# Optimization experiments

Hardware: AMD Instinct MI355X
Metric: run time of the kernel (lower is better)

Reference implementation:

```python
import jax, jax.numpy as jnp
import numpy as np

STRIDE = 16.0
PRE_NMS_TOP_N = 6000
POST_NMS_TOP_N = 1000
NMS_THRESH = 0.7
MIN_SIZE = 0.0
BBOX_XFORM_CLIP = float(np.log(1000.0 / 16.0))

# ---- Detectron-style anchor generation (numpy, setup-time only) ----

def _whctrs(a):
    w = a[2] - a[0] + 1
    h = a[3] - a[1] + 1
    return w, h, a[0] + 0.5 * (w - 1), a[1] + 0.5 * (h - 1)

def _mkanchors(ws, hs, xc, yc):
    return np.stack([xc - 0.5 * (ws - 1), yc - 0.5 * (hs - 1),
                     xc + 0.5 * (ws - 1), yc + 0.5 * (hs - 1)], axis=1)

def _ratio_enum(a, ratios):
    w, h, xc, yc = _whctrs(a)
    size = w * h
    ws = np.round(np.sqrt(size / ratios))
    hs = np.round(ws * ratios)
    return _mkanchors(ws, hs, xc, yc)

def _scale_enum(a, scales):
    w, h, xc, yc = _whctrs(a)
    return _mkanchors(w * scales, h * scales, xc, yc)

def generate_anchors(stride=16.0, sizes=(32, 64, 128, 256, 512), aspect_ratios=(0.5, 1.0, 2.0)):
    scales = np.array(sizes, dtype=np.float64) / stride
    ratios = np.array(aspect_ratios, dtype=np.float64)
    base = np.array([1, 1, stride, stride], dtype=np.float64) - 1
    ra = _ratio_enum(base, ratios)
    return np.vstack([_scale_enum(ra[i], scales) for i in range(ra.shape[0])]).astype(np.float32)


def conv2d(x, w, b, pad):
    y = jax.lax.conv_general_dilated(x, w, (1, 1), [(pad, pad), (pad, pad)],
                                     dimension_numbers=('NCHW', 'OIHW', 'NCHW'))
    return y + b[None, :, None, None]


def _proposals_one(scores, deltas, iminfo, anchors):
    # scores: (A,H,W) sigmoid probs; deltas: (4A,H,W); iminfo: [im_h, im_w, im_scale]
    A, H, W = scores.shape
    gx, gy = jnp.meshgrid(jnp.arange(W, dtype=scores.dtype) * STRIDE,
                          jnp.arange(H, dtype=scores.dtype) * STRIDE)
    shifts = jnp.stack([gx, gy, gx, gy], axis=-1)  # (H,W,4)
    all_anchors = (shifts[:, :, None, :] + anchors[None, None]).reshape(-1, 4)  # (H*W*A,4)
    sc = scores.transpose(1, 2, 0).reshape(-1)      # (H*W*A,)  anchor-minor, matches Detectron
    dl = deltas.transpose(1, 2, 0).reshape(-1, 4)   # (H*W*A,4)

    top_sc, idx = jax.lax.top_k(sc, PRE_NMS_TOP_N)  # descending scores
    boxes = all_anchors[idx]
    d = dl[idx]

    # bbox_transform decode (weights = 1)
    widths = boxes[:, 2] - boxes[:, 0] + 1.0
    heights = boxes[:, 3] - boxes[:, 1] + 1.0
    ctr_x = boxes[:, 0] + 0.5 * widths
    ctr_y = boxes[:, 1] + 0.5 * heights
    dx, dy = d[:, 0], d[:, 1]
    dw = jnp.minimum(d[:, 2], BBOX_XFORM_CLIP)
    dh = jnp.minimum(d[:, 3], BBOX_XFORM_CLIP)
    pcx = dx * widths + ctr_x
    pcy = dy * heights + ctr_y
    pw = jnp.exp(dw) * widths
    ph = jnp.exp(dh) * heights
    x1 = pcx - 0.5 * pw
    y1 = pcy - 0.5 * ph
    x2 = pcx + 0.5 * pw - 1.0
    y2 = pcy + 0.5 * ph - 1.0

    im_h, im_w, im_scale = iminfo[0], iminfo[1], iminfo[2]
    x1 = jnp.clip(x1, 0.0, im_w - 1.0)
    y1 = jnp.clip(y1, 0.0, im_h - 1.0)
    x2 = jnp.clip(x2, 0.0, im_w - 1.0)
    y2 = jnp.clip(y2, 0.0, im_h - 1.0)

    ws = x2 - x1 + 1.0
    hs = y2 - y1 + 1.0
    xc = x1 + ws / 2.0
    yc = y1 + hs / 2.0
    ms = MIN_SIZE * im_scale
    valid = (ws >= ms) & (hs >= ms) & (xc < im_w) & (yc < im_h)

    boxes_s = jnp.stack([x1, y1, x2, y2], axis=1)

    # greedy NMS over score-sorted boxes (invalid boxes start suppressed)
    areas = ws * hs
    ix1 = jnp.maximum(x1[:, None], x1[None, :])
    iy1 = jnp.maximum(y1[:, None], y1[None, :])
    ix2 = jnp.minimum(x2[:, None], x2[None, :])
    iy2 = jnp.minimum(y2[:, None], y2[None, :])
    iw = jnp.maximum(ix2 - ix1 + 1.0, 0.0)
    ih = jnp.maximum(iy2 - iy1 + 1.0, 0.0)
    inter = iw * ih
    iou = inter / (areas[:, None] + areas[None, :] - inter)

    N = PRE_NMS_TOP_N
    rng = jnp.arange(N)

    def body(i, keep):
        sup = (iou[i] > NMS_THRESH) & (rng > i)
        return jnp.where(keep[i], keep & ~sup, keep)

    keep = jax.lax.fori_loop(0, N, body, valid)

    final_sc = jnp.where(keep, jnp.where(valid, top_sc, -1.0), -1.0)
    out_sc, kidx = jax.lax.top_k(final_sc, POST_NMS_TOP_N)
    out_boxes = boxes_s[kidx]
    return out_boxes, out_sc


def setup_inputs() -> dict:
    key = jax.random.key(0)
    ks = jax.random.split(key, 5)
    B, C, H, W = 2, 512, 50, 84
    A = 15  # 5 sizes x 3 aspect ratios
    x = jax.random.normal(ks[0], (B, C, H, W), jnp.float32)
    conv_w = 0.01 * jax.random.normal(ks[1], (C, C, 3, 3), jnp.float32)
    conv_b = jnp.zeros((C,), jnp.float32)
    cls_w = 0.01 * jax.random.normal(ks[2], (A, C, 1, 1), jnp.float32)
    cls_b = jnp.zeros((A,), jnp.float32)
    bbox_w = 0.01 * jax.random.normal(ks[3], (4 * A, C, 1, 1), jnp.float32)
    bbox_b = jnp.zeros((4 * A,), jnp.float32)
    anchors = jnp.asarray(generate_anchors(STRIDE))
    im_info = jnp.array([[800.0, 1333.0, 1.6], [800.0, 1333.0, 1.6]], jnp.float32)
    return {'x': x, 'im_info': im_info, 'conv_w': conv_w, 'conv_b': conv_b,
            'cls_w': cls_w, 'cls_b': cls_b, 'bbox_w': bbox_w, 'bbox_b': bbox_b,
            'anchors': anchors}


def reference(x, im_info, conv_w, conv_b, cls_w, cls_b, bbox_w, bbox_b, anchors):
    h = jax.nn.relu(conv2d(x, conv_w, conv_b, 1))
    rpn_cls_logits = conv2d(h, cls_w, cls_b, 0)        # (B, A, H, W)
    rpn_bbox_pred = conv2d(h, bbox_w, bbox_b, 0)       # (B, 4A, H, W)
    rpn_cls_prob = jax.nn.sigmoid(rpn_cls_logits)      # CLS_ACTIVATION = 'sigmoid'
    boxes, probs = jax.vmap(_proposals_one, in_axes=(0, 0, 0, None))(
        rpn_cls_prob, rpn_bbox_pred, im_info, anchors)  # (B, POST_NMS, 4), (B, POST_NMS)
    B = x.shape[0]
    bidx = jnp.broadcast_to(jnp.arange(B, dtype=boxes.dtype)[:, None, None],
                            (B, POST_NMS_TOP_N, 1))
    rpn_rois = jnp.concatenate([bidx, boxes], axis=-1)  # (B, POST_NMS, 5)
    return rpn_cls_logits, rpn_bbox_pred, rpn_rois, probs
```

## Files before the change

### kernel.cpp

```cpp
#include <hip/hip_runtime.h>
#include <cstdint>
#include <cstddef>

typedef unsigned long long u64;
typedef unsigned int u32;

constexpr int B_ = 2, C_ = 512, H_ = 50, W_ = 84, A_ = 15;
constexpr int HW_ = H_ * W_;
constexpr int NS_ = HW_ * A_;
constexpr int PRE_ = 6000, POST_ = 1000;
constexpr int WORDS_ = 94;
constexpr int NPAD_ = 6016;
constexpr int SORTN_ = 8192;
constexpr double NMS_T = 0.7;
constexpr double CLIP_ = 4.1351665567423556;
constexpr int OUT_ROIS_ = B_ * A_ * HW_ + B_ * 4 * A_ * HW_;
constexpr int OUT_PROBS_ = OUT_ROIS_ + B_ * POST_ * 5;
constexpr int NROUNDS_ = 5;

__global__ void k_init(const float* __restrict__ w, double* __restrict__ wt64,
                       double* __restrict__ h0, double* __restrict__ h1,
                       double* __restrict__ h2, double* __restrict__ h3, int nbuf,
                       u64* __restrict__ mask, u32* __restrict__ selcnt,
                       u32* __restrict__ selhist, u64* __restrict__ selk,
                       u32* __restrict__ seli) {
  int idx = blockIdx.x * 256 + threadIdx.x;
  if (idx < C_ * C_ * 9) {
    int co = idx & 511;
    int r = idx >> 9;
    int k = r % 9;
    int ci = r / 9;
    wt64[idx] = (double)w[(co * C_ + ci) * 9 + k];
  }
  if (idx < B_ * C_ * HW_) {
    h0[idx] = 0.0; h1[idx] = 0.0;
    if (nbuf == 4) { h2[idx] = 0.0; h3[idx] = 0.0; }
  }
  if (idx < B_ * NPAD_ * WORDS_) mask[idx] = 0ull;
  if (idx < 2) selcnt[idx] = 0u;
  if (idx < NROUNDS_ * 2 * 256) selhist[idx] = 0u;
  if (idx < B_ * SORTN_) { selk[idx] = 0ull; seli[idx] = 0xFFFFFFFFu; }
}

template<int QBITS>
__global__ __launch_bounds__(256) void k_conv3(const float* __restrict__ x,
                                               const double* __restrict__ wt64,
                                               double* __restrict__ h0,
                                               double* __restrict__ h1,
                                               double* __restrict__ h2,
                                               double* __restrict__ h3) {
  constexpr int CHUNKS = 128 >> QBITS;
  const int tid = threadIdx.x;
  const int lane = tid & 63;
  const int wid = __builtin_amdgcn_readfirstlane(tid >> 6);
  const int cg = lane % 12;
  const int rowg = lane / 12;
  const bool act = (rowg < 5);
  const int colb = blockIdx.x;
  const int rowb = blockIdx.y;
  const int z = blockIdx.z;
  const int b = z >> (4 + QBITS);
  const int cob = (z >> QBITS) & 15;
  const int q = z & ((1 << QBITS) - 1);
  const int c0 = colb * 12;
  const int rblk = rowb * 10;
  const int col = c0 + cg;
  const int rg5 = act ? rowg : 4;
  const int r0 = rblk + rg5 * 2;
  const int cstart = q * CHUNKS;
  const int bsel = q >> 1;
  double* __restrict__ hp = (bsel == 0) ? h0 : (bsel == 1) ? h1 : (bsel == 2) ? h2 : h3;

  __shared__ double xs[4][14][14];

  double acc[2][8];
#pragma unroll
  for (int j = 0; j < 2; ++j)
#pragma unroll
    for (int c = 0; c < 8; ++c) acc[j][c] = 0.0;

  float xreg[3];
  auto loadX = [&](int cb4) {
#pragma unroll
    for (int k = 0; k < 3; ++k) {
      int s = tid + k * 256;
      float v = 0.f;
      if (s < 672) {
        int ci = s / 168;
        int r168 = s % 168;
        int rr = r168 / 14;
        int cc = r168 % 14;
        int gr = rblk - 1 + rr, gc = c0 - 1 + cc;
        if (gr >= 0 && gr < H_ && gc >= 0 && gc < W_)
          v = x[((b * C_ + cb4 * 4 + ci) * H_ + gr) * W_ + gc];
      }
      xreg[k] = v;
    }
  };
  auto storeX = [&]() {
#pragma unroll
    for (int k = 0; k < 3; ++k) {
      int s = tid + k * 256;
      if (s < 672) {
        int ci = s / 168;
        int r168 = s % 168;
        int rr = r168 / 14;
        int cc = r168 % 14;
        xs[ci][cc][rr] = (double)xreg[k];
      }
    }
  };

  const double* __restrict__ wb = wt64 + (size_t)(cob * 32 + wid * 8);

  loadX(cstart);
  for (int it = 0; it < CHUNKS; ++it) {
    const int cb4 = cstart + it;
    __syncthreads();
    storeX();
    __syncthreads();
    if (it < CHUNKS - 1) loadX(cb4 + 1);
#pragma unroll
    for (int ci = 0; ci < 4; ++ci) {
#pragma unroll
      for (int kx = 0; kx < 3; ++kx) {
        double xv[4];
        const double* xp = &xs[ci][cg + kx][rg5 * 2];
#pragma unroll
        for (int t = 0; t < 4; ++t) xv[t] = xp[t];
#pragma unroll
        for (int ky = 0; ky < 3; ++ky) {
          const double* __restrict__ wp =
              wb + ((size_t)(cb4 * 4 + ci) * 9 + (ky * 3 + kx)) * C_;
#pragma unroll
          for (int c = 0; c < 8; ++c) {
            double wv = wp[c];
            acc[0][c] = fma(xv[ky], wv, acc[0][c]);
            acc[1][c] = fma(xv[ky + 1], wv, acc[1][c]);
          }
        }
      }
    }
  }

  if (act) {
#pragma unroll
    for (int c = 0; c < 8; ++c) {
      int co = cob * 32 + wid * 8 + c;
#pragma unroll
      for (int j = 0; j < 2; ++j) {
        atomicAdd(&hp[((size_t)b * C_ + co) * HW_ + (r0 + j) * W_ + col], acc[j][c]);
      }
    }
  }
}

__global__ __launch_bounds__(256) void k_conv1(const double* __restrict__ h0,
                                               const double* __restrict__ h1,
                                               const double* __restrict__ h2,
                                               const double* __restrict__ h3, int nbuf,
                                               const float* __restrict__ convb,
                                               const float* __restrict__ clsw,
                                               const float* __restrict__ clsb,
                                               const float* __restrict__ bbw,
                                               const float* __restrict__ bbb,
                                               float* __restrict__ out,
                                               double* __restrict__ scores,
                                               double* __restrict__ deltas) {
  const int b = blockIdx.y;
  const int p0 = blockIdx.x * 32;
  const int tid = threadIdx.x;
  const int px = tid & 31, cg = tid >> 5;
  __shared__ double hs[64][32];
  __shared__ double wl[64][80];
  double acc[10];
#pragma unroll
  for (int k = 0; k < 10; ++k) acc[k] = 0.0;
  for (int ci0 = 0; ci0 < C_; ci0 += 64) {
    for (int s = tid; s < 64 * 32; s += 256) {
      int ci = s >> 5, pp = s & 31;
      int p = p0 + pp;
      double v = 0.0;
      if (p < HW_) {
        size_t idx = ((size_t)b * C_ + ci0 + ci) * HW_ + p;
        double hsum = h0[idx] + h1[idx];
        if (nbuf == 4) hsum = hsum + (h2[idx] + h3[idx]);
        v = hsum + (double)convb[ci0 + ci];
        v = v > 0.0 ? v : 0.0;
      }
      hs[ci][pp] = v;
    }
    for (int s = tid; s < 64 * 80; s += 256) {
      int ci = s / 80, c = s % 80;
      double v = 0.0;
      if (c < 15) v = (double)clsw[c * C_ + ci0 + ci];
      else if (c < 75) v = (double)bbw[(c - 15) * C_ + ci0 + ci];
      wl[ci][c] = v;
    }
    __syncthreads();
    for (int ci = 0; ci < 64; ++ci) {
      double xv = hs[ci][px];
#pragma unroll
      for (int k = 0; k < 10; ++k)
        acc[k] = fma(wl[ci][cg * 10 + k], xv, acc[k]);
    }
    __syncthreads();
  }
  int p = p0 + px;
  if (p < HW_) {
#pragma unroll
    for (int k = 0; k < 10; ++k) {
      int c = cg * 10 + k;
      if (c < 15) {
        double z = acc[k] + (double)clsb[c];
        out[(size_t)b * NS_ + c * HW_ + p] = (float)z;
        double s = 1.0 / (1.0 + exp(-z));
        scores[(size_t)b * NS_ + (size_t)p * A_ + c] = s;
      } else if (c < 75) {
        int cbx = c - 15;
        double z = acc[k] + (double)bbb[cbx];
        out[(size_t)B_ * NS_ + (size_t)b * (4 * A_ * HW_) + cbx * HW_ + p] = (float)z;
        deltas[(size_t)b * (4 * NS_) + (size_t)p * (4 * A_) + cbx] = z;
      }
    }
  }
}

__device__ inline u64 compute_prefix(const u32* __restrict__ selhist, int b, int rounds) {
  u64 prefix = 0;
  u32 above = 0;
  for (int rr = 0; rr < rounds; ++rr) {
    const u32* h = selhist + (rr * 2 + b) * 256;
    int shift = 56 - 8 * rr;
    u32 c = above;
    int dsel = 0;
    for (int dd = 255; dd >= 0; --dd) {
      u32 nc = c + h[dd];
      if (nc >= (u32)PRE_) { dsel = dd; break; }
      c = nc;
    }
    prefix |= ((u64)dsel << shift);
    above = c;
  }
  return prefix;
}

__global__ __launch_bounds__(256) void k_hist(const double* __restrict__ scores,
                                              u32* __restrict__ selhist, int r) {
  const int b = blockIdx.y;
  const double* sc = scores + (size_t)b * NS_;
  const int lane = (int)(threadIdx.x & 63);
  const int shift = 56 - 8 * r;
  __shared__ u64 sh_prefix;
  if (threadIdx.x == 0) sh_prefix = (r == 0) ? 0ull : compute_prefix(selhist, b, r);
  __syncthreads();
  const u64 prefix = sh_prefix;
  const u64 himask = (r == 0) ? 0ull : (~0ull << (shift + 8));
  u32* hist = selhist + (r * 2 + b) * 256;
  for (int i = blockIdx.x * 256 + (int)threadIdx.x; i < NS_; i += 64 * 256) {
    u64 k = (u64)__double_as_longlong(sc[i]);
    bool valid = ((k & himask) == (prefix & himask));
    u32 d = (u32)((k >> shift) & 255);
    u64 m = __ballot(valid);
#pragma unroll
    for (int bit = 0; bit < 8; ++bit) {
      u64 bb = __ballot((d >> bit) & 1);
      m &= ((d >> bit) & 1) ? bb : ~bb;
    }
    if (valid && lane == (__ffsll((unsigned long long)m) - 1))
      atomicAdd(&hist[d], (u32)__popcll(m));
  }
}

__global__ __launch_bounds__(256) void k_compact(const double* __restrict__ scores,
                                                 const u32* __restrict__ selhist,
                                                 u32* __restrict__ selcnt,
                                                 u64* __restrict__ selk,
                                                 u32* __restrict__ seli) {
  const int b = blockIdx.y;
  const double* sc = scores + (size_t)b * NS_;
  const int lane = (int)(threadIdx.x & 63);
  __shared__ u64 sh_T;
  if (threadIdx.x == 0) sh_T = compute_prefix(selhist, b, NROUNDS_);
  __syncthreads();
  const u64 T = sh_T;
  for (int i = blockIdx.x * 256 + (int)threadIdx.x; i < NS_; i += 64 * 256) {
    u64 k = (u64)__double_as_longlong(sc[i]);
    bool q = (k >= T);
    u64 bal = __ballot(q);
    if (bal) {
      int leader = __ffsll((unsigned long long)bal) - 1;
      u32 wbase = 0;
      if (lane == leader) wbase = atomicAdd(&selcnt[b], (u32)__popcll(bal));
      wbase = (u32)__shfl((int)wbase, leader);
      if (q) {
        u64 below = (lane == 0) ? 0ull : (~0ull >> (64 - lane));
        u32 pos = wbase + (u32)__popcll(bal & below);
        if (pos < (u32)SORTN_) {
          selk[(size_t)b * SORTN_ + pos] = k;
          seli[(size_t)b * SORTN_ + pos] = (u32)i;
        }
      }
    }
  }
}

__global__ __launch_bounds__(1024) void k_sort(const u64* __restrict__ selk,
                                               const u32* __restrict__ seli,
                                               double* __restrict__ ssc,
                                               u32* __restrict__ sidx) {
  const int b = blockIdx.x;
  __shared__ u64 kk[SORTN_];
  __shared__ u32 vv[SORTN_];
  for (int i = threadIdx.x; i < SORTN_; i += 1024) {
    kk[i] = selk[(size_t)b * SORTN_ + i];
    vv[i] = seli[(size_t)b * SORTN_ + i];
  }
  __syncthreads();
  for (int k = 2; k <= SORTN_; k <<= 1) {
    for (int j = k >> 1; j > 0; j >>= 1) {
      for (int t = threadIdx.x; t < SORTN_; t += 1024) {
        int ixj = t ^ j;
        if (ixj > t) {
          u64 ka = kk[t], kb2 = kk[ixj];
          u32 va = vv[t], vb = vv[ixj];
          bool aBetter = (ka > kb2) || (ka == kb2 && va < vb);
          bool bBetter = (kb2 > ka) || (kb2 == ka && vb < va);
          bool up = (t & k) == 0;
          bool sw = up ? bBetter : aBetter;
          if (sw) {
            kk[t] = kb2; kk[ixj] = ka;
            vv[t] = vb;  vv[ixj] = va;
          }
        }
      }
      __syncthreads();
    }
  }
  for (int i = threadIdx.x; i < PRE_; i += 1024) {
    ssc[(size_t)b * PRE_ + i] = __longlong_as_double((long long)kk[i]);
    sidx[(size_t)b * PRE_ + i] = vv[i];
  }
}

__global__ __launch_bounds__(256) void k_decode(const u32* __restrict__ sidx,
                                                const double* __restrict__ deltas,
                                                const float* __restrict__ anchors,
                                                const float* __restrict__ iminfo,
                                                double* __restrict__ boxes,
                                                double* __restrict__ areas,
                                                u64* __restrict__ vmask) {
#pragma clang fp contract(off)
  const int b = blockIdx.y;
  const int i = blockIdx.x * 256 + (int)threadIdx.x;
  bool valid = false;
  if (i < NPAD_) {
    double x1 = 0, y1 = 0, x2 = 0, y2 = 0, ar = 0;
    if (i < PRE_) {
      u32 idx = sidx[(size_t)b * PRE_ + i];
      int p = (int)idx / A_, a = (int)idx % A_;
      int yy = p / W_, xx = p % W_;
      double sx = xx * 16.0, sy = yy * 16.0;
      double b0 = sx + (double)anchors[a * 4 + 0];
      double b1 = sy + (double)anchors[a * 4 + 1];
      double b2 = sx + (double)anchors[a * 4 + 2];
      double b3 = sy + (double)anchors[a * 4 + 3];
      double wdt = b2 - b0 + 1.0, hgt = b3 - b1 + 1.0;
      double cx = b0 + 0.5 * wdt, cy = b1 + 0.5 * hgt;
      const double* d = deltas + (size_t)b * (4 * NS_) + (size_t)idx * 4;
      double dx = d[0], dy = d[1];
      double dw = d[2] < CLIP_ ? d[2] : CLIP_;
      double dh = d[3] < CLIP_ ? d[3] : CLIP_;
      double pcx = dx * wdt + cx, pcy = dy * hgt + cy;
      double pw = exp(dw) * wdt, ph = exp(dh) * hgt;
      x1 = pcx - 0.5 * pw;
      y1 = pcy - 0.5 * ph;
      x2 = pcx + 0.5 * pw - 1.0;
      y2 = pcy + 0.5 * ph - 1.0;
      double imh = (double)iminfo[b * 3 + 0];
      double imw = (double)iminfo[b * 3 + 1];
      x1 = x1 < 0.0 ? 0.0 : (x1 > imw - 1.0 ? imw - 1.0 : x1);
      y1 = y1 < 0.0 ? 0.0 : (y1 > imh - 1.0 ? imh - 1.0 : y1);
      x2 = x2 < 0.0 ? 0.0 : (x2 > imw - 1.0 ? imw - 1.0 : x2);
      y2 = y2 < 0.0 ? 0.0 : (y2 > imh - 1.0 ? imh - 1.0 : y2);
      double wss = x2 - x1 + 1.0, hss = y2 - y1 + 1.0;
      double xc = x1 + wss / 2.0, yc = y1 + hss / 2.0;
      valid = (wss >= 0.0) && (hss >= 0.0) && (xc < imw) && (yc < imh);
      ar = wss * hss;
    }
    double* bx = boxes + ((size_t)b * NPAD_ + i) * 4;
    bx[0] = x1; bx[1] = y1; bx[2] = x2; bx[3] = y2;
    areas[(size_t)b * NPAD_ + i] = ar;
  }
  u64 bal = __ballot(valid);
  if ((threadIdx.x & 63) == 0) {
    int w = i >> 6;
    if (w < WORDS_) vmask[b * WORDS_ + w] = bal;
  }
}

__global__ __launch_bounds__(256) void k_mask(const double* __restrict__ boxes,
                                              const double* __restrict__ areas,
                                              u64* __restrict__ mask) {
#pragma clang fp contract(off)
  const int b = blockIdx.z;
  const int wc = blockIdx.x;
  const int rq = blockIdx.y;
  if (wc * 64 + 63 <= rq * 256) return;
  const int i = rq * 256 + (int)threadIdx.x;
  __shared__ double cbx[64][4];
  __shared__ double car[64];
  if (threadIdx.x < 64) {
    int sj = wc * 64 + (int)threadIdx.x;
    const double* pj = boxes + ((size_t)b * NPAD_ + sj) * 4;
    cbx[threadIdx.x][0] = pj[0];
    cbx[threadIdx.x][1] = pj[1];
    cbx[threadIdx.x][2] = pj[2];
    cbx[threadIdx.x][3] = pj[3];
    car[threadIdx.x] = areas[(size_t)b * NPAD_ + sj];
  }
  __syncthreads();
  if (i >= PRE_) return;
  int jmax = PRE_ - wc * 64;
  if (jmax > 64) jmax = 64;
  if (wc * 64 + jmax - 1 <= i) return;
  const double* bi = boxes + ((size_t)b * NPAD_ + i) * 4;
  double x1 = bi[0], y1 = bi[1], x2 = bi[2], y2 = bi[3];
  double ai = areas[(size_t)b * NPAD_ + i];
  u64 m = 0;
  for (int j2 = 0; j2 < jmax; ++j2) {
    int j = wc * 64 + j2;
    if (j > i) {
      double ix1 = x1 > cbx[j2][0] ? x1 : cbx[j2][0];
      double iy1 = y1 > cbx[j2][1] ? y1 : cbx[j2][1];
      double ix2 = x2 < cbx[j2][2] ? x2 : cbx[j2][2];
      double iy2 = y2 < cbx[j2][3] ? y2 : cbx[j2][3];
      double iw = ix2 - ix1 + 1.0;
      if (iw < 0.0) iw = 0.0;
      double ih = iy2 - iy1 + 1.0;
      if (ih < 0.0) ih = 0.0;
      double inter = iw * ih;
      double iou = inter / (ai + car[j2] - inter);
      if (iou > NMS_T) m |= (1ull << j2);
    }
  }
  if (m) mask[((size_t)b * NPAD_ + i) * WORDS_ + wc] = m;
}

__global__ __launch_bounds__(64) void k_scan(const u64* __restrict__ mask,
                                             const u64* __restrict__ vmask,
                                             u64* __restrict__ keepm) {
  const int b = blockIdx.x;
  const int lane = (int)threadIdx.x;
  u64 rem0 = ~vmask[b * WORDS_ + lane];
  u64 rem1 = (lane < WORDS_ - 64) ? ~vmask[b * WORDS_ + 64 + lane] : ~0ull;
  const u64* mb = mask + (size_t)b * NPAD_ * WORDS_;
  int kept = 0;
  int Bb = 0;
  u64 dgnext = (lane < 64) ? mb[(size_t)lane * WORDS_ + 0] : 0ull;
  for (; Bb < WORDS_ && kept < POST_; ++Bb) {
    const int base = Bb * 64;
    int lim = PRE_ - base;
    if (lim > 64) lim = 64;
    u64 dg = (lane < lim) ? dgnext : 0ull;
    if (Bb + 1 < WORDS_) {
      int nbase = (Bb + 1) * 64;
      int nlim = PRE_ - nbase;
      if (nlim > 64) nlim = 64;
      dgnext = (lane < nlim) ? mb[(size_t)(nbase + lane) * WORDS_ + (Bb + 1)] : 0ull;
    }
    u64 cur = (Bb < 64) ? __shfl(rem0, Bb) : __shfl(rem1, Bb - 64);
    if (lim < 64) cur |= (~0ull) << lim;
    u64 kb = 0;
    while (cur != ~0ull) {
      int t = __ffsll((unsigned long long)~cur) - 1;
      kb |= 1ull << t;
      cur |= __shfl(dg, t);
      cur |= 1ull << t;
      if (++kept >= POST_) break;
    }
    u64 or0 = 0, or1 = 0;
    u64 k2 = kb;
    while (k2) {
      int t0 = __ffsll((unsigned long long)k2) - 1; k2 &= k2 - 1;
      int t1 = -1, t2 = -1, t3 = -1;
      if (k2) { t1 = __ffsll((unsigned long long)k2) - 1; k2 &= k2 - 1; }
      if (k2) { t2 = __ffsll((unsigned long long)k2) - 1; k2 &= k2 - 1; }
      if (k2) { t3 = __ffsll((unsigned long long)k2) - 1; k2 &= k2 - 1; }
      const u64* m0 = mb + (size_t)(base + t0) * WORDS_;
      u64 a0 = m0[lane];
      u64 a1 = (lane < WORDS_ - 64) ? m0[64 + lane] : 0ull;
      u64 b0 = 0, b1 = 0, c0 = 0, c1 = 0, d0 = 0, d1 = 0;
      if (t1 >= 0) {
        const u64* m1 = mb + (size_t)(base + t1) * WORDS_;
        b0 = m1[lane]; b1 = (lane < WORDS_ - 64) ? m1[64 + lane] : 0ull;
      }
      if (t2 >= 0) {
        const u64* m2 = mb + (size_t)(base + t2) * WORDS_;
        c0 = m2[lane]; c1 = (lane < WORDS_ - 64) ? m2[64 + lane] : 0ull;
      }
      if (t3 >= 0) {
        const u64* m3 = mb + (size_t)(base + t3) * WORDS_;
        d0 = m3[lane]; d1 = (lane < WORDS_ - 64) ? m3[64 + lane] : 0ull;
      }
      or0 |= (a0 | b0) | (c0 | d0);
      or1 |= (a1 | b1) | (c1 | d1);
    }
    rem0 |= or0;
    rem1 |= or1;
    if (lane == 0) keepm[b * WORDS_ + Bb] = kb;
  }
  for (int w = Bb + lane; w < WORDS_; w += 64)
    keepm[b * WORDS_ + w] = 0ull;
}

__global__ __launch_bounds__(256) void k_final(const u64* __restrict__ keepm,
                                               const double* __restrict__ boxes,
                                               const double* __restrict__ ssc,
                                               float* __restrict__ out) {
  const int b = blockIdx.x;
  __shared__ u32 pk[WORDS_ + 1];
  __shared__ u64 km_s[WORDS_];
  for (int w = threadIdx.x; w < WORDS_; w += 256) km_s[w] = keepm[b * WORDS_ + w];
  __syncthreads();
  if (threadIdx.x == 0) {
    u32 a = 0;
    for (int w = 0; w < WORDS_; ++w) {
      pk[w] = a;
      a += (u32)__popcll(km_s[w]);
    }
    pk[WORDS_] = a;
  }
  __syncthreads();
  const u32 K = pk[WORDS_];
  for (int i = threadIdx.x; i < PRE_; i += 256) {
    int w = i >> 6, t = i & 63;
    u64 km = km_s[w];
    u32 before = pk[w] + (u32)__popcll(km & ((1ull << t) - 1ull));
    bool kp = (km >> t) & 1ull;
    int slot = kp ? (int)before : (int)K + (i - (int)before);
    if (slot < POST_) {
      const double* bx = boxes + ((size_t)b * NPAD_ + i) * 4;
      float* ro = out + OUT_ROIS_ + ((size_t)b * POST_ + slot) * 5;
      ro[0] = (float)b;
      ro[1] = (float)bx[0];
      ro[2] = (float)bx[1];
      ro[3] = (float)bx[2];
      ro[4] = (float)bx[3];
      out[OUT_PROBS_ + b * POST_ + slot] = kp ? (float)ssc[(size_t)b * PRE_ + i] : -1.0f;
    }
  }
}

extern "C" void kernel_launch(void* const* d_in, const int* in_sizes, int n_in,
                              void* d_out, int out_size, void* d_ws, size_t ws_size,
                              hipStream_t stream) {
  (void)in_sizes; (void)n_in; (void)out_size;
  const float* x = (const float*)d_in[0];
  const float* iminfo = (const float*)d_in[1];
  const float* convw = (const float*)d_in[2];
  const float* convb = (const float*)d_in[3];
  const float* clsw = (const float*)d_in[4];
  const float* clsb = (const float*)d_in[5];
  const float* bbw = (const float*)d_in[6];
  const float* bbb = (const float*)d_in[7];
  const float* anchors = (const float*)d_in[8];
  float* out = (float*)d_out;

  char* ws = (char*)d_ws;
  size_t off = 0;
  auto alloc = [&](size_t bytes) -> void* {
    void* p = ws + off;
    off += (bytes + 255) & ~(size_t)255;
    return p;
  };
  const size_t HB = (size_t)B_ * C_ * HW_ * 8;
  double* wt64 = (double*)alloc((size_t)C_ * 9 * C_ * 8);
  double* h0 = (double*)alloc(HB);
  double* h1 = (double*)alloc(HB);
  double* scores = (double*)alloc((size_t)B_ * NS_ * 8);
  double* deltas = (double*)alloc((size_t)B_ * NS_ * 4 * 8);
  u64* selk = (u64*)alloc((size_t)B_ * SORTN_ * 8);
  u32* seli = (u32*)alloc((size_t)B_ * SORTN_ * 4);
  double* ssc = (double*)alloc((size_t)B_ * PRE_ * 8);
  u32* sidx = (u32*)alloc((size_t)B_ * PRE_ * 4);
  double* boxes = (double*)alloc((size_t)B_ * NPAD_ * 4 * 8);
  double* areas = (double*)alloc((size_t)B_ * NPAD_ * 8);
  u64* vmask = (u64*)alloc((size_t)B_ * WORDS_ * 8);
  u64* mask = (u64*)alloc((size_t)B_ * NPAD_ * WORDS_ * 8);
  u64* keepm = (u64*)alloc((size_t)B_ * WORDS_ * 8);
  u32* selcnt = (u32*)alloc(2 * 4);
  u32* selhist = (u32*)alloc((size_t)NROUNDS_ * 2 * 256 * 4);

  const bool k8 = (ws_size >= off + 2 * (HB + 256) + 256);
  double* h2 = h0;
  double* h3 = h1;
  int nbuf = 2;
  if (k8) {
    h2 = (double*)alloc(HB);
    h3 = (double*)alloc(HB);
    nbuf = 4;
  }

  k_init<<<(B_ * C_ * HW_ + 255) / 256, 256, 0, stream>>>(
      convw, wt64, h0, h1, h2, h3, nbuf, mask, selcnt, selhist, selk, seli);
  if (k8)
    k_conv3<3><<<dim3(7, 5, 256), 256, 0, stream>>>(x, wt64, h0, h1, h2, h3);
  else
    k_conv3<2><<<dim3(7, 5, 128), 256, 0, stream>>>(x, wt64, h0, h1, h2, h3);
  k_conv1<<<dim3(132, 2), 256, 0, stream>>>(h0, h1, h2, h3, nbuf, convb, clsw, clsb,
                                            bbw, bbb, out, scores, deltas);
  for (int r = 0; r < NROUNDS_; ++r)
    k_hist<<<dim3(64, 2), 256, 0, stream>>>(scores, selhist, r);
  k_compact<<<dim3(64, 2), 256, 0, stream>>>(scores, selhist, selcnt, selk, seli);
  k_sort<<<2, 1024, 0, stream>>>(selk, seli, ssc, sidx);
  k_decode<<<dim3(24, 2), 256, 0, stream>>>(sidx, deltas, anchors, iminfo, boxes, areas, vmask);
  k_mask<<<dim3(94, 24, 2), 256, 0, stream>>>(boxes, areas, mask);
  k_scan<<<2, 64, 0, stream>>>(mask, vmask, keepm);
  k_final<<<2, 256, 0, stream>>>(keepm, boxes, ssc, out);
}
```

Measured before the change: 1.494 ms.

## Replace single-block bitonic sort with parallel rank-counting sort and scatter

The top-K selection sort, which ran as a bitonic sort in one 1024-thread block per image, is replaced by a rank-counting sort. Each candidate's rank is computed by comparing it against a chunk of all other candidates, spread over 8x8 blocks per image, with partial counts combined by atomics and then scattered to sorted positions. This trades a serial-dependent sort on two CUs for more total O(n^2) comparisons spread across many CUs, and it drops the selk/seli padding initialisation.

Result: faster. 1.385 ms (-7.3%).

```diff
diff --git a/kernel.cpp b/kernel.cpp
--- a/kernel.cpp
+++ b/kernel.cpp
@@ -17,13 +17,13 @@
 constexpr int OUT_ROIS_ = B_ * A_ * HW_ + B_ * 4 * A_ * HW_;
 constexpr int OUT_PROBS_ = OUT_ROIS_ + B_ * POST_ * 5;
 constexpr int NROUNDS_ = 5;
+constexpr int JCH_ = 8;
 
 __global__ void k_init(const float* __restrict__ w, double* __restrict__ wt64,
                        double* __restrict__ h0, double* __restrict__ h1,
                        double* __restrict__ h2, double* __restrict__ h3, int nbuf,
                        u64* __restrict__ mask, u32* __restrict__ selcnt,
-                       u32* __restrict__ selhist, u64* __restrict__ selk,
-                       u32* __restrict__ seli) {
+                       u32* __restrict__ selhist, u32* __restrict__ rankb) {
   int idx = blockIdx.x * 256 + threadIdx.x;
   if (idx < C_ * C_ * 9) {
     int co = idx & 511;
@@ -39,7 +39,7 @@
   if (idx < B_ * NPAD_ * WORDS_) mask[idx] = 0ull;
   if (idx < 2) selcnt[idx] = 0u;
   if (idx < NROUNDS_ * 2 * 256) selhist[idx] = 0u;
-  if (idx < B_ * SORTN_) { selk[idx] = 0ull; seli[idx] = 0xFFFFFFFFu; }
+  if (idx < B_ * SORTN_) rankb[idx] = 0u;
 }
 
 template<int QBITS>
@@ -305,41 +305,64 @@
   }
 }
 
-__global__ __launch_bounds__(1024) void k_sort(const u64* __restrict__ selk,
-                                               const u32* __restrict__ seli,
-                                               double* __restrict__ ssc,
-                                               u32* __restrict__ sidx) {
-  const int b = blockIdx.x;
-  __shared__ u64 kk[SORTN_];
-  __shared__ u32 vv[SORTN_];
-  for (int i = threadIdx.x; i < SORTN_; i += 1024) {
-    kk[i] = selk[(size_t)b * SORTN_ + i];
-    vv[i] = seli[(size_t)b * SORTN_ + i];
-  }
-  __syncthreads();
-  for (int k = 2; k <= SORTN_; k <<= 1) {
-    for (int j = k >> 1; j > 0; j >>= 1) {
-      for (int t = threadIdx.x; t < SORTN_; t += 1024) {
-        int ixj = t ^ j;
-        if (ixj > t) {
-          u64 ka = kk[t], kb2 = kk[ixj];
-          u32 va = vv[t], vb = vv[ixj];
-          bool aBetter = (ka > kb2) || (ka == kb2 && va < vb);
-          bool bBetter = (kb2 > ka) || (kb2 == ka && vb < va);
-          bool up = (t & k) == 0;
-          bool sw = up ? bBetter : aBetter;
-          if (sw) {
-            kk[t] = kb2; kk[ixj] = ka;
-            vv[t] = vb;  vv[ixj] = va;
-          }
-        }
-      }
-      __syncthreads();
-    }
-  }
-  for (int i = threadIdx.x; i < PRE_; i += 1024) {
-    ssc[(size_t)b * PRE_ + i] = __longlong_as_double((long long)kk[i]);
-    sidx[(size_t)b * PRE_ + i] = vv[i];
+__global__ __launch_bounds__(1024) void k_rankcnt(const u64* __restrict__ selk,
+                                                  const u32* __restrict__ seli,
+                                                  const u32* __restrict__ selcnt,
+                                                  u32* __restrict__ rankb) {
+  const int b = blockIdx.z;
+  int mn = (int)selcnt[b];
+  if (mn > SORTN_) mn = SORTN_;
+  const int e = blockIdx.x * 1024 + (int)threadIdx.x;
+  const bool active = (e < mn);
+  u64 ke = 0; u32 ie = 0;
+  if (active) {
+    ke = selk[(size_t)b * SORTN_ + e];
+    ie = seli[(size_t)b * SORTN_ + e];
+  }
+  const int jlen = (mn + JCH_ - 1) / JCH_;
+  const int j0 = blockIdx.y * jlen;
+  int j1 = j0 + jlen;
+  if (j1 > mn) j1 = mn;
+  __shared__ u64 ks[1024];
+  __shared__ u32 isx[1024];
+  u32 cnt = 0;
+  for (int t0 = j0; t0 < j1; t0 += 1024) {
+    int j = t0 + (int)threadIdx.x;
+    if (j < j1) {
+      ks[threadIdx.x] = selk[(size_t)b * SORTN_ + j];
+      isx[threadIdx.x] = seli[(size_t)b * SORTN_ + j];
+    }
+    __syncthreads();
+    int lim = j1 - t0;
+    if (lim > 1024) lim = 1024;
+    if (active) {
+      for (int jj = 0; jj < lim; ++jj) {
+        u64 kj = ks[jj];
+        bool better = (kj > ke) || (kj == ke && isx[jj] < ie);
+        cnt += better ? 1u : 0u;
+      }
+    }
+    __syncthreads();
+  }
+  if (active && cnt) atomicAdd(&rankb[b * SORTN_ + e], cnt);
+}
+
+__global__ __launch_bounds__(256) void k_scatter(const u64* __restrict__ selk,
+                                                 const u32* __restrict__ seli,
+                                                 const u32* __restrict__ selcnt,
+                                                 const u32* __restrict__ rankb,
+                                                 double* __restrict__ ssc,
+                                                 u32* __restrict__ sidx) {
+  const int b = blockIdx.y;
+  int mn = (int)selcnt[b];
+  if (mn > SORTN_) mn = SORTN_;
+  int e = blockIdx.x * 256 + (int)threadIdx.x;
+  if (e < mn) {
+    u32 r = rankb[b * SORTN_ + e];
+    if (r < (u32)PRE_) {
+      ssc[(size_t)b * PRE_ + r] = __longlong_as_double((long long)selk[(size_t)b * SORTN_ + e]);
+      sidx[(size_t)b * PRE_ + r] = seli[(size_t)b * SORTN_ + e];
+    }
   }
 }
 
@@ -591,6 +614,7 @@
   u64* keepm = (u64*)alloc((size_t)B_ * WORDS_ * 8);
   u32* selcnt = (u32*)alloc(2 * 4);
   u32* selhist = (u32*)alloc((size_t)NROUNDS_ * 2 * 256 * 4);
+  u32* rankb = (u32*)alloc((size_t)B_ * SORTN_ * 4);
 
   const bool k8 = (ws_size >= off + 2 * (HB + 256) + 256);
   double* h2 = h0;
@@ -603,7 +627,7 @@
   }
 
   k_init<<<(B_ * C_ * HW_ + 255) / 256, 256, 0, stream>>>(
-      convw, wt64, h0, h1, h2, h3, nbuf, mask, selcnt, selhist, selk, seli);
+      convw, wt64, h0, h1, h2, h3, nbuf, mask, selcnt, selhist, rankb);
   if (k8)
     k_conv3<3><<<dim3(7, 5, 256), 256, 0, stream>>>(x, wt64, h0, h1, h2, h3);
   else
@@ -613,7 +637,8 @@
   for (int r = 0; r < NROUNDS_; ++r)
     k_hist<<<dim3(64, 2), 256, 0, stream>>>(scores, selhist, r);
   k_compact<<<dim3(64, 2), 256, 0, stream>>>(scores, selhist, selcnt, selk, seli);
-  k_sort<<<2, 1024, 0, stream>>>(selk, seli, ssc, sidx);
+  k_rankcnt<<<dim3(8, JCH_, 2), 1024, 0, stream>>>(selk, seli, selcnt, rankb);
+  k_scatter<<<dim3(32, 2), 256, 0, stream>>>(selk, seli, selcnt, rankb, ssc, sidx);
   k_decode<<<dim3(24, 2), 256, 0, stream>>>(sidx, deltas, anchors, iminfo, boxes, areas, vmask);
   k_mask<<<dim3(94, 24, 2), 256, 0, stream>>>(boxes, areas, mask);
   k_scan<<<2, 64, 0, stream>>>(mask, vmask, keepm);
```
